# Performance work log

Measured on AMD Instinct MI355X. Metric: run time of the kernel, lower is better.

Reference implementation:

```python
import jax, jax.numpy as jnp
import numpy as np
import math

D = 256; H = 8; L = 6; DK = D // H

def _ln(x, g, b):
    m = jnp.mean(x, -1, keepdims=True)
    v = jnp.mean((x - m) ** 2, -1, keepdims=True)
    return (x - m) * jax.lax.rsqrt(v + 1e-5) * g + b

def setup_inputs() -> dict:
    key = jax.random.key(0)
    ks = jax.random.split(key, 16)
    B, N, F, E = 8, 768, 128, 4
    s = 0.02
    inp = {}
    inp['node_feats'] = jax.random.normal(ks[0], (B, N, F), jnp.float32)
    inp['adj'] = jax.random.randint(ks[1], (B, N, N), 0, 2, jnp.int32)
    inp['dist'] = jax.random.uniform(ks[2], (B, N, N), jnp.float32)
    inp['edge_type_oh'] = jax.random.uniform(ks[3], (B, N, N, E), jnp.float32)
    inp['node_proj_w'] = jax.random.normal(ks[4], (F, D), jnp.float32) * s
    inp['node_proj_b'] = jnp.zeros((D,), jnp.float32)
    inp['cls'] = jax.random.normal(ks[5], (1, 1, D), jnp.float32) * s
    inp['etw'] = jax.random.normal(ks[6], (E,), jnp.float32) * s
    inp['noedge_bias'] = jnp.float32(-2.0)
    inp['deg_scale'] = jnp.float32(0.2)
    inp['gamma'] = jnp.float32(0.8)
    inp['v2n'] = jnp.float32(0.1)
    inp['n2v'] = jnp.float32(0.1)
    inp['vself'] = jnp.float32(0.05)
    inp['ln1_g'] = jnp.ones((L, D), jnp.float32); inp['ln1_b'] = jnp.zeros((L, D), jnp.float32)
    inp['qw'] = jax.random.normal(ks[7], (L, D, D), jnp.float32) * s; inp['qb'] = jnp.zeros((L, D), jnp.float32)
    inp['kw'] = jax.random.normal(ks[8], (L, D, D), jnp.float32) * s; inp['kb'] = jnp.zeros((L, D), jnp.float32)
    inp['vw'] = jax.random.normal(ks[9], (L, D, D), jnp.float32) * s; inp['vb'] = jnp.zeros((L, D), jnp.float32)
    inp['ow'] = jax.random.normal(ks[10], (L, D, D), jnp.float32) * s; inp['ob'] = jnp.zeros((L, D), jnp.float32)
    inp['ln2_g'] = jnp.ones((L, D), jnp.float32); inp['ln2_b'] = jnp.zeros((L, D), jnp.float32)
    Dm = int(D * 1.0)  # mlp_ratio=1.0
    inp['fc1w'] = jax.random.normal(ks[11], (L, D, Dm), jnp.float32) * s; inp['fc1b'] = jnp.zeros((L, Dm), jnp.float32)
    inp['fc2w'] = jax.random.normal(ks[12], (L, Dm, D), jnp.float32) * s; inp['fc2b'] = jnp.zeros((L, D), jnp.float32)
    return inp

def _build_bias(adj_f, dist, edge_type_oh, etw, noedge_bias, deg_scale, gamma, v2n, n2v, vself):
    # DynamicAttnBiasBuilder: hard_mask=False, use_degree=True, vnode_spd_mode='replace', gamma != 0
    B, N, _ = adj_f.shape
    T = N + 1
    e = jnp.einsum('bije,e->bij', edge_type_oh, etw) - gamma * dist  # (B,N,N)
    e = jnp.where(adj_f > 0, e, e + noedge_bias)
    deg = adj_f.sum(-1)  # (B,N)
    deg_norm = (deg[:, :, None] + deg[:, None, :]) / (deg.max(axis=1, keepdims=True)[:, :, None] + 1e-6)
    e = e + deg_scale * deg_norm
    bias = jnp.zeros((B, T, T), jnp.float32)
    bias = bias.at[:, 1:, 1:].set(e)
    bias = bias.at[:, 0, 1:].set(v2n)   # vnode_spd_mode == 'replace'
    bias = bias.at[:, 1:, 0].set(n2v)
    bias = bias.at[:, 0, 0].set(vself)
    return bias  # (B,T,T), broadcast over heads

def _mhsa(x, bias, qw, qb, kw, kb, vw, vb, ow, ob):
    B, T, _ = x.shape
    q = (x @ qw + qb).reshape(B, T, H, DK).transpose(0, 2, 1, 3)
    k = (x @ kw + kb).reshape(B, T, H, DK).transpose(0, 2, 1, 3)
    v = (x @ vw + vb).reshape(B, T, H, DK).transpose(0, 2, 1, 3)
    scores = jnp.einsum('bhqd,bhkd->bhqk', q, k) / math.sqrt(DK)
    scores = scores + bias[:, None, :, :]
    attn = jax.nn.softmax(scores, axis=-1)
    out = jnp.einsum('bhqk,bhkd->bhqd', attn, v)
    out = out.transpose(0, 2, 1, 3).reshape(B, T, D)
    return out @ ow + ob

def _forward(node_feats, adj, dist, edge_type_oh, node_proj_w, node_proj_b, cls,
             etw, noedge_bias, deg_scale, gamma, v2n, n2v, vself,
             ln1_g, ln1_b, qw, qb, kw, kb, vw, vb, ow, ob,
             ln2_g, ln2_b, fc1w, fc1b, fc2w, fc2b):
    adj_f = adj.astype(jnp.float32)
    bias = _build_bias(adj_f, dist, edge_type_oh, etw, noedge_bias, deg_scale, gamma, v2n, n2v, vself)
    B = node_feats.shape[0]
    x = node_feats @ node_proj_w + node_proj_b  # (B,N,D)
    x = jnp.concatenate([jnp.broadcast_to(cls, (B, 1, D)), x], axis=1)  # prepend virtual node -> (B,T,D)
    for l in range(L):
        h = _mhsa(_ln(x, ln1_g[l], ln1_b[l]), bias, qw[l], qb[l], kw[l], kb[l], vw[l], vb[l], ow[l], ob[l])
        x = x + h
        m = _ln(x, ln2_g[l], ln2_b[l])
        m = jax.nn.gelu(m @ fc1w[l] + fc1b[l], approximate=False) @ fc2w[l] + fc2b[l]
        x = x + m
    return x

def reference(node_feats, adj, dist, edge_type_oh, node_proj_w, node_proj_b, cls,
              etw, noedge_bias, deg_scale, gamma, v2n, n2v, vself,
              ln1_g, ln1_b, qw, qb, kw, kb, vw, vb, ow, ob,
              ln2_g, ln2_b, fc1w, fc1b, fc2w, fc2b):
    return _forward(node_feats, adj, dist, edge_type_oh, node_proj_w, node_proj_b, cls,
                    etw, noedge_bias, deg_scale, gamma, v2n, n2v, vself,
                    ln1_g, ln1_b, qw, qb, kw, kb, vw, vb, ow, ob,
                    ln2_g, ln2_b, fc1w, fc1b, fc2w, fc2b)
```

## Files before the change

kernel.cpp:

```cpp
#include <hip/hip_runtime.h>
#include <math.h>

#define BB 8
#define NN 768
#define TT 769
#define DD 256
#define HH 8
#define DKK 32
#define FF 128
#define LL 6
#define MM 6152
#define SCALE 0.17677669529663687f
#define TP 832
#define KQP 784
#define KHS (KQP * DKK)
#define GBP 776
#define HP 264
#define WSZ 65536
#define NPK ((size_t)BB * 49 * 13 * 1024)

typedef __attribute__((ext_vector_type(8))) short s16x8;
typedef __attribute__((ext_vector_type(8))) unsigned short u16x8;
typedef __attribute__((ext_vector_type(4))) float f32x4;

__device__ inline short f2bf(float x) {
    unsigned u = __float_as_uint(x);
    unsigned r = (u + 0x7FFFu + ((u >> 16) & 1u)) >> 16;
    return (short)r;
}
__device__ inline float bf2f(unsigned short s) {
    return __uint_as_float(((unsigned)s) << 16);
}
__device__ inline float gelu_f(float x) {
    return 0.5f * x * (1.f + erff(x * 0.70710678118654752f));
}

__global__ __launch_bounds__(256) void deg_kernel(const int* __restrict__ adj,
                                                  float* __restrict__ deg) {
    int row  = blockIdx.x * 4 + (threadIdx.x >> 6);
    int lane = threadIdx.x & 63;
    const int* p = adj + (size_t)row * NN;
    int s = 0;
#pragma unroll
    for (int i = 0; i < NN / 64; ++i) s += p[lane + 64 * i];
#pragma unroll
    for (int off = 32; off > 0; off >>= 1) s += __shfl_xor(s, off);
    if (lane == 0) deg[row] = (float)s;
}

__global__ __launch_bounds__(256) void degmax_kernel(const float* __restrict__ deg,
                                                     float* __restrict__ dmax) {
    __shared__ float red[256];
    int b = blockIdx.x, t = threadIdx.x;
    float m = 0.f;
    for (int i = t; i < NN; i += 256) m = fmaxf(m, deg[b * NN + i]);
    red[t] = m;
    __syncthreads();
    for (int s = 128; s > 0; s >>= 1) {
        if (t < s) red[t] = fmaxf(red[t], red[t + s]);
        __syncthreads();
    }
    if (t == 0) dmax[b] = red[0];
}

__global__ __launch_bounds__(256) void bias_kernel(
    const float* __restrict__ dist, const float* __restrict__ eoh,
    const int* __restrict__ adj, const float* __restrict__ deg,
    const float* __restrict__ dmax, const float* __restrict__ etw,
    const float* __restrict__ noedge, const float* __restrict__ degsc,
    const float* __restrict__ gamma, const float* __restrict__ v2n,
    const float* __restrict__ n2v, const float* __restrict__ vself,
    unsigned short* __restrict__ bias)
{
    long long idx = (long long)blockIdx.x * 256 + threadIdx.x;
    const long long total = (long long)BB * TT * GBP;
    if (idx >= total) return;
    int b  = (int)(idx / ((long long)TT * GBP));
    int r  = (int)(idx % ((long long)TT * GBP));
    int qi = r / GBP, kj = r % GBP;
    float out;
    if (kj >= TT)                out = 0.f;
    else if (qi == 0 && kj == 0) out = vself[0];
    else if (qi == 0)            out = v2n[0];
    else if (kj == 0)            out = n2v[0];
    else {
        int i = qi - 1, j = kj - 1;
        size_t e = ((size_t)b * NN + i) * NN + j;
        float4 oh = *(const float4*)(eoh + 4 * e);
        float val = oh.x * etw[0] + oh.y * etw[1] + oh.z * etw[2] + oh.w * etw[3]
                    - gamma[0] * dist[e];
        if (adj[e] == 0) val += noedge[0];
        val += degsc[0] * (deg[b * NN + i] + deg[b * NN + j]) / (dmax[b] + 1e-6f);
        out = val;
    }
    bias[idx] = (unsigned short)f2bf(out);
}

__global__ __launch_bounds__(256) void biaspk_kernel(
    const unsigned short* __restrict__ bias, unsigned short* __restrict__ bpk)
{
    int idx = blockIdx.x * 256 + threadIdx.x;
    int jj   = idx & 7;
    int lane = (idx >> 3) & 63;
    int half = (idx >> 9) & 1;
    int c    = (idx >> 10) % 13;
    int qtb  = idx / (13 * 1024);
    int b = qtb / 49, qt = qtb - b * 49;
    int quad = lane >> 4, m16 = lane & 15;
    int j = half * 8 + jj, s = j >> 2, r = j & 3;
    int kj = c * 64 + s * 16 + m16; if (kj >= TT) kj = 0;
    int qi = qt * 16 + quad * 4 + r; if (qi >= TT) qi = TT - 1;
    bpk[idx] = bias[(size_t)(b * TT + qi) * GBP + kj];
}

__global__ __launch_bounds__(256) void nodeproj_ln_kernel(
    const float* __restrict__ nf, const float* __restrict__ w,
    const float* __restrict__ bsv, const float* __restrict__ cls,
    const float* __restrict__ g, const float* __restrict__ bvec,
    float* __restrict__ x, short* __restrict__ xn)
{
    __shared__ float sf[FF];
    __shared__ float red[256];
    int row = blockIdx.x, t = threadIdx.x;
    int b = row / TT, tr = row % TT;
    float y;
    if (tr == 0) {
        y = cls[t];
    } else {
        if (t < FF) sf[t] = nf[((size_t)b * NN + tr - 1) * FF + t];
        __syncthreads();
        y = bsv[t];
#pragma unroll 8
        for (int kk = 0; kk < FF; ++kk) y = fmaf(sf[kk], w[kk * DD + t], y);
    }
    x[(size_t)row * DD + t] = y;
    red[t] = y;
    __syncthreads();
    for (int s = 128; s > 0; s >>= 1) { if (t < s) red[t] += red[t + s]; __syncthreads(); }
    float mean = red[0] * (1.f / DD);
    __syncthreads();
    float d = y - mean;
    red[t] = d * d;
    __syncthreads();
    for (int s = 128; s > 0; s >>= 1) { if (t < s) red[t] += red[t + s]; __syncthreads(); }
    float var = red[0] * (1.f / DD);
    xn[(size_t)row * DD + t] = f2bf(d * rsqrtf(var + 1e-5f) * g[t] + bvec[t]);
}

__global__ __launch_bounds__(256) void wtrans_kernel(
    const float* __restrict__ qw, const float* __restrict__ kw,
    const float* __restrict__ vw, const float* __restrict__ ow,
    const float* __restrict__ f1w, const float* __restrict__ f2w,
    short* __restrict__ wt2)
{
    int mi = blockIdx.x >> 4, kg = blockIdx.x & 15;
    int fam = mi / 6, l = mi % 6;
    const float* W;
    if      (fam == 0) W = qw;
    else if (fam == 1) W = kw;
    else if (fam == 2) W = vw;
    else if (fam == 3) W = ow;
    else if (fam == 4) W = f1w;
    else               W = f2w;
    W += (size_t)l * DD * DD;
    int n = threadIdx.x;
    short* out = wt2 + (size_t)mi * WSZ;
#pragma unroll
    for (int kk = 0; kk < 16; ++kk) {
        int k = kg * 16 + kk;
        float val = W[(size_t)k * DD + n];
        size_t idx = (size_t)(((n >> 4) * 8 + (k >> 5)) * 512
                   + (((k >> 3) & 3) * 16 + (n & 15)) * 8 + (k & 7));
        out[idx] = f2bf(val);
    }
}

__global__ __launch_bounds__(256) void gemm_qkv_kernel(
    const short* __restrict__ A, const short* __restrict__ wtl,
    const float* __restrict__ qb, const float* __restrict__ kb,
    const float* __restrict__ vb,
    short* __restrict__ qh, short* __restrict__ kh, short* __restrict__ vtb)
{
    int t = threadIdx.x;
    int w = t >> 6, lane = t & 63, quad = lane >> 4, m16 = lane & 15;
    int m0 = blockIdx.x * 16;
    int fam = blockIdx.y;
    const short* Wf = wtl + (size_t)fam * 6 * WSZ;
    const float* bsv = fam == 0 ? qb : (fam == 1 ? kb : vb);
    int arow = m0 + m16; if (arow >= MM) arow = MM - 1;
    const short* ap = A + (size_t)arow * DD + quad * 8;
    const short* wbase = Wf + (size_t)(w * 4) * 4096 + lane * 8;
    f32x4 acc[4] = {};
#pragma unroll
    for (int kc = 0; kc < 8; ++kc) {
        s16x8 af = *(const s16x8*)(ap + kc * 32);
#pragma unroll
        for (int nt = 0; nt < 4; ++nt) {
            s16x8 bf = *(const s16x8*)(wbase + (size_t)nt * 4096 + kc * 512);
            acc[nt] = __builtin_amdgcn_mfma_f32_16x16x32_bf16(af, bf, acc[nt], 0, 0, 0);
        }
    }
    if (fam < 2) {
        short* outp = fam == 0 ? qh : kh;
#pragma unroll
        for (int r = 0; r < 4; ++r) {
            int row = m0 + quad * 4 + r;
            if (row < MM) {
                int b = row / TT;
                int tpos = row - b * TT;
                size_t rb = ((size_t)b * HH * KQP + tpos) * DKK;
#pragma unroll
                for (int nt = 0; nt < 4; ++nt) {
                    int col = w * 64 + nt * 16 + m16;
                    float bv = bsv[col];
                    int h = col >> 5, dk = col & 31;
                    outp[rb + (size_t)h * KHS + dk] = f2bf(acc[nt][r] + bv);
                }
            }
        }
    } else {
#pragma unroll
        for (int nt = 0; nt < 4; ++nt) {
            int col = w * 64 + nt * 16 + m16;
            float bv = bsv[col];
            int h = col >> 5, dk = col & 31;
#pragma unroll
            for (int r = 0; r < 4; ++r) {
                int row = m0 + quad * 4 + r;
                if (row < MM) {
                    int b = row / TT;
                    int tpos = row - b * TT;
                    vtb[(((size_t)(b * HH + h)) * DKK + dk) * TP + tpos] =
                        f2bf(acc[nt][r] + bv);
                }
            }
        }
    }
}

__global__ __launch_bounds__(512) void mega_kernel(
    const short* __restrict__ q, const short* __restrict__ k,
    const short* __restrict__ vt, const unsigned short* __restrict__ bpk,
    const short* __restrict__ Wo, const short* __restrict__ W1,
    const short* __restrict__ W2,
    const float* __restrict__ ob, const float* __restrict__ g2,
    const float* __restrict__ b2, const float* __restrict__ f1b,
    const float* __restrict__ f2b, float* __restrict__ x,
    short* __restrict__ xn, const float* __restrict__ g1,
    const float* __restrict__ b1, int donext)
{
    __shared__ short Pb[8][16][72];
    __shared__ short xa[16][HP];
    __shared__ short xnl[16][HP];
    __shared__ short hb[16][HP];
    __shared__ float redS[16][8], redQ[16][8];

    int t = threadIdx.x;
    int w = t >> 6, lane = t & 63;
    int quad = lane >> 4, m16 = lane & 15;
    int bx = blockIdx.x;
    int b = bx / 49;
    int qt = bx - b * 49;
    int h = w;
    int q0 = qt * 16;
    size_t qtb13 = (size_t)(b * 49 + qt) * 13;

    int qrow = q0 + m16;
    int qc = qrow < TT ? qrow : TT - 1;
    const short* qbase = q + (size_t)(b * HH + h) * KHS;
    s16x8 qa = *(const s16x8*)(qbase + (size_t)qc * DKK + quad * 8);

    const short* kbase = k + (size_t)(b * HH + h) * KHS;
    const short* vbase = vt + (((size_t)(b * HH + h)) * DKK) * TP;

    s16x8 kfA[4], kfB[4], vfA[4], vfB[4];
    u16x8 bbA0, bbA1, bbB0, bbB1;
    f32x4 sacc[4];
    f32x4 o0 = {0.f, 0.f, 0.f, 0.f};
    f32x4 o1 = {0.f, 0.f, 0.f, 0.f};
    float ls[4] = {0.f, 0.f, 0.f, 0.f};

#define LOADK_(DST, CC)                                                         \
    {                                                                           \
        _Pragma("unroll") for (int s = 0; s < 4; ++s) {                         \
            int kr = (CC) * 64 + s * 16 + m16;                                  \
            int kcl = kr < TT ? kr : TT - 1;                                    \
            DST[s] = *(const s16x8*)(kbase + (size_t)kcl * DKK + quad * 8);     \
        }                                                                       \
    }
#define LOADV_(DST, CC)                                                         \
    {                                                                           \
        int jn = (CC) * 64;                                                     \
        DST[0] = *(const s16x8*)(vbase + (size_t)m16 * TP + jn + quad * 8);     \
        DST[1] = *(const s16x8*)(vbase + (size_t)m16 * TP + jn + 32 + quad * 8);\
        DST[2] = *(const s16x8*)(vbase + (size_t)(16 + m16) * TP + jn + quad * 8);\
        DST[3] = *(const s16x8*)(vbase + (size_t)(16 + m16) * TP + jn + 32 + quad * 8);\
    }
#define LOADB_(D0, D1, CC)                                                      \
    {                                                                           \
        const unsigned short* bp_ = bpk + ((qtb13 + (CC)) << 10);               \
        D0 = *(const u16x8*)(bp_ + (lane << 3));                                \
        D1 = *(const u16x8*)(bp_ + 512 + (lane << 3));                          \
    }
#define STEP_(C, KPRE, KUSE, VUSE, VPRE, BU0, BU1, BP0, BP1, PK, PV, PBF, DOQK) \
    {                                                                           \
        if (PK)  LOADK_(KPRE, (C) + 2);                                         \
        if (PV)  LOADV_(VPRE, (C) + 1);                                         \
        if (PBF) LOADB_(BP0, BP1, (C) + 1);                                     \
        int j0 = (C) * 64;                                                      \
        _Pragma("unroll") for (int s = 0; s < 4; ++s) {                         \
            int key = j0 + s * 16 + m16;                                        \
            int kv = key < TT;                                                  \
            _Pragma("unroll") for (int r = 0; r < 4; ++r) {                     \
                int j = s * 4 + r;                                              \
                float bv = bf2f(j < 8 ? (unsigned short)BU0[j]                  \
                                      : (unsigned short)BU1[j - 8]);            \
                float sval = kv ? fmaf(sacc[s][r], SCALE, bv) : -1e30f;         \
                float p = __expf(sval - 8.0f);                                  \
                ls[r] += p;                                                     \
                Pb[w][quad * 4 + r][s * 16 + m16] = f2bf(p);                    \
            }                                                                   \
        }                                                                       \
        if (DOQK) {                                                             \
            f32x4 z = {0.f, 0.f, 0.f, 0.f};                                     \
            _Pragma("unroll") for (int s = 0; s < 4; ++s)                       \
                sacc[s] = __builtin_amdgcn_mfma_f32_16x16x32_bf16(qa, KUSE[s], z, 0, 0, 0); \
        }                                                                       \
        s16x8 pa0 = *(const s16x8*)&Pb[w][m16][quad * 8];                       \
        s16x8 pa1 = *(const s16x8*)&Pb[w][m16][32 + quad * 8];                  \
        o0 = __builtin_amdgcn_mfma_f32_16x16x32_bf16(pa0, VUSE[0], o0, 0, 0, 0);\
        o0 = __builtin_amdgcn_mfma_f32_16x16x32_bf16(pa1, VUSE[1], o0, 0, 0, 0);\
        o1 = __builtin_amdgcn_mfma_f32_16x16x32_bf16(pa0, VUSE[2], o1, 0, 0, 0);\
        o1 = __builtin_amdgcn_mfma_f32_16x16x32_bf16(pa1, VUSE[3], o1, 0, 0, 0);\
    }

    LOADK_(kfA, 0);
    LOADK_(kfB, 1);
    LOADV_(vfA, 0);
    LOADB_(bbA0, bbA1, 0);
    {
        f32x4 z = {0.f, 0.f, 0.f, 0.f};
#pragma unroll
        for (int s = 0; s < 4; ++s)
            sacc[s] = __builtin_amdgcn_mfma_f32_16x16x32_bf16(qa, kfA[s], z, 0, 0, 0);
    }

    for (int cc = 0; cc < 5; ++cc) {
        STEP_(2 * cc,     kfA, kfB, vfA, vfB, bbA0, bbA1, bbB0, bbB1, 1, 1, 1, 1)
        STEP_(2 * cc + 1, kfB, kfA, vfB, vfA, bbB0, bbB1, bbA0, bbA1, 1, 1, 1, 1)
    }
    STEP_(10, kfA, kfB, vfA, vfB, bbA0, bbA1, bbB0, bbB1, 1, 1, 1, 1)
    STEP_(11, kfB, kfA, vfB, vfA, bbB0, bbB1, bbA0, bbA1, 0, 1, 1, 1)
    STEP_(12, kfA, kfB, vfA, vfB, bbA0, bbA1, bbB0, bbB1, 0, 0, 0, 0)

#undef STEP_
#undef LOADB_
#undef LOADV_
#undef LOADK_

#pragma unroll
    for (int r = 0; r < 4; ++r) {
        float l = ls[r];
#pragma unroll
        for (int off = 1; off < 16; off <<= 1) l += __shfl_xor(l, off);
        float inv = 1.f / l;
        int rl = quad * 4 + r;
        xa[rl][h * DKK + m16]      = f2bf(o0[r] * inv);
        xa[rl][h * DKK + 16 + m16] = f2bf(o1[r] * inv);
    }
    __syncthreads();

    const short* wob = Wo + (size_t)(w * 2) * 4096 + lane * 8;
    f32x4 acco[2] = {};
#pragma unroll
    for (int kc = 0; kc < 8; ++kc) {
        s16x8 af = *(const s16x8*)&xa[m16][kc * 32 + quad * 8];
#pragma unroll
        for (int ntl = 0; ntl < 2; ++ntl) {
            s16x8 bf = *(const s16x8*)(wob + (size_t)ntl * 4096 + kc * 512);
            acco[ntl] = __builtin_amdgcn_mfma_f32_16x16x32_bf16(af, bf, acco[ntl], 0, 0, 0);
        }
    }
    float vv[2][4], sr[4], q2[4];
#pragma unroll
    for (int r = 0; r < 4; ++r) { sr[r] = 0.f; q2[r] = 0.f; }
#pragma unroll
    for (int ntl = 0; ntl < 2; ++ntl) {
        int col = w * 32 + ntl * 16 + m16;
        float bv = ob[col];
#pragma unroll
        for (int r = 0; r < 4; ++r) {
            int row = q0 + quad * 4 + r; if (row >= TT) row = TT - 1;
            float v = acco[ntl][r] + bv + x[((size_t)(b * TT + row)) * DD + col];
            vv[ntl][r] = v; sr[r] += v; q2[r] += v * v;
        }
    }
#pragma unroll
    for (int r = 0; r < 4; ++r)
#pragma unroll
        for (int off = 1; off < 16; off <<= 1) {
            sr[r] += __shfl_xor(sr[r], off);
            q2[r] += __shfl_xor(q2[r], off);
        }
    if (m16 == 0) {
#pragma unroll
        for (int r = 0; r < 4; ++r) {
            redS[quad * 4 + r][w] = sr[r];
            redQ[quad * 4 + r][w] = q2[r];
        }
    }
    __syncthreads();

#pragma unroll
    for (int r = 0; r < 4; ++r) {
        int rl = quad * 4 + r;
        float fs = 0.f, fq = 0.f;
#pragma unroll
        for (int j = 0; j < 8; ++j) { fs += redS[rl][j]; fq += redQ[rl][j]; }
        float mean = fs * (1.f / DD);
        float var = fq * (1.f / DD) - mean * mean;
        float inv = rsqrtf(var + 1e-5f);
#pragma unroll
        for (int ntl = 0; ntl < 2; ++ntl) {
            int col = w * 32 + ntl * 16 + m16;
            xnl[rl][col] = f2bf((vv[ntl][r] - mean) * inv * g2[col] + b2[col]);
        }
    }
    __syncthreads();

    const short* w1b = W1 + (size_t)(w * 2) * 4096 + lane * 8;
    f32x4 acc1[2] = {};
#pragma unroll
    for (int kc = 0; kc < 8; ++kc) {
        s16x8 af = *(const s16x8*)&xnl[m16][kc * 32 + quad * 8];
#pragma unroll
        for (int ntl = 0; ntl < 2; ++ntl) {
            s16x8 bf = *(const s16x8*)(w1b + (size_t)ntl * 4096 + kc * 512);
            acc1[ntl] = __builtin_amdgcn_mfma_f32_16x16x32_bf16(af, bf, acc1[ntl], 0, 0, 0);
        }
    }
#pragma unroll
    for (int ntl = 0; ntl < 2; ++ntl) {
        int col = w * 32 + ntl * 16 + m16;
        float fb = f1b[col];
#pragma unroll
        for (int r = 0; r < 4; ++r)
            hb[quad * 4 + r][col] = f2bf(gelu_f(acc1[ntl][r] + fb));
    }
    __syncthreads();

    const short* w2b = W2 + (size_t)(w * 2) * 4096 + lane * 8;
    f32x4 acc2[2] = {};
#pragma unroll
    for (int kc = 0; kc < 8; ++kc) {
        s16x8 af = *(const s16x8*)&hb[m16][kc * 32 + quad * 8];
#pragma unroll
        for (int ntl = 0; ntl < 2; ++ntl) {
            s16x8 bf = *(const s16x8*)(w2b + (size_t)ntl * 4096 + kc * 512);
            acc2[ntl] = __builtin_amdgcn_mfma_f32_16x16x32_bf16(af, bf, acc2[ntl], 0, 0, 0);
        }
    }
#pragma unroll
    for (int r = 0; r < 4; ++r) { sr[r] = 0.f; q2[r] = 0.f; }
#pragma unroll
    for (int ntl = 0; ntl < 2; ++ntl) {
        int col = w * 32 + ntl * 16 + m16;
        float bv = f2b[col];
#pragma unroll
        for (int r = 0; r < 4; ++r) {
            float v = acc2[ntl][r] + bv + vv[ntl][r];
            vv[ntl][r] = v; sr[r] += v; q2[r] += v * v;
        }
    }
#pragma unroll
    for (int r = 0; r < 4; ++r)
#pragma unroll
        for (int off = 1; off < 16; off <<= 1) {
            sr[r] += __shfl_xor(sr[r], off);
            q2[r] += __shfl_xor(q2[r], off);
        }
    if (m16 == 0) {
#pragma unroll
        for (int r = 0; r < 4; ++r) {
            redS[quad * 4 + r][w] = sr[r];
            redQ[quad * 4 + r][w] = q2[r];
        }
    }
    __syncthreads();

#pragma unroll
    for (int r = 0; r < 4; ++r) {
        int rl = quad * 4 + r;
        int row = q0 + rl;
        float fs = 0.f, fq = 0.f;
#pragma unroll
        for (int j = 0; j < 8; ++j) { fs += redS[rl][j]; fq += redQ[rl][j]; }
        float mean = fs * (1.f / DD);
        float var = fq * (1.f / DD) - mean * mean;
        float inv = rsqrtf(var + 1e-5f);
        if (row < TT) {
            size_t grow = (size_t)(b * TT + row) * DD;
#pragma unroll
            for (int ntl = 0; ntl < 2; ++ntl) {
                int col = w * 32 + ntl * 16 + m16;
                float v = vv[ntl][r];
                x[grow + col] = v;
                if (donext)
                    xn[grow + col] = f2bf((v - mean) * inv * g1[col] + b1[col]);
            }
        }
    }
}

extern "C" void kernel_launch(void* const* d_in, const int* in_sizes, int n_in,
                              void* d_out, int out_size, void* d_ws, size_t ws_size,
                              hipStream_t stream)
{
    const float* node_feats = (const float*)d_in[0];
    const int*   adj        = (const int*)d_in[1];
    const float* dist       = (const float*)d_in[2];
    const float* eoh        = (const float*)d_in[3];
    const float* npw        = (const float*)d_in[4];
    const float* npb        = (const float*)d_in[5];
    const float* cls        = (const float*)d_in[6];
    const float* etw        = (const float*)d_in[7];
    const float* noedge     = (const float*)d_in[8];
    const float* degsc      = (const float*)d_in[9];
    const float* gamma      = (const float*)d_in[10];
    const float* v2n        = (const float*)d_in[11];
    const float* n2v        = (const float*)d_in[12];
    const float* vself      = (const float*)d_in[13];
    const float* ln1g = (const float*)d_in[14];
    const float* ln1b = (const float*)d_in[15];
    const float* qw   = (const float*)d_in[16];
    const float* qb   = (const float*)d_in[17];
    const float* kw   = (const float*)d_in[18];
    const float* kb   = (const float*)d_in[19];
    const float* vw   = (const float*)d_in[20];
    const float* vb   = (const float*)d_in[21];
    const float* ow   = (const float*)d_in[22];
    const float* ob   = (const float*)d_in[23];
    const float* ln2g = (const float*)d_in[24];
    const float* ln2b = (const float*)d_in[25];
    const float* f1w  = (const float*)d_in[26];
    const float* f1b  = (const float*)d_in[27];
    const float* f2w  = (const float*)d_in[28];
    const float* f2b  = (const float*)d_in[29];

    float* x  = (float*)d_out;
    char* ws = (char*)d_ws;
    size_t off = 0;
    unsigned short* bias = (unsigned short*)(ws + off); off += (size_t)BB * TT * GBP * 2;
    unsigned short* bpk  = (unsigned short*)(ws + off); off += NPK * 2;
    float* deg  = (float*)(ws + off); off += (size_t)BB * NN * 4;
    float* dmax = (float*)(ws + off); off += 64;
    short* xn16 = (short*)(ws + off); off += (size_t)MM * DD * 2;
    short* qhb  = (short*)(ws + off); off += (size_t)BB * HH * KQP * DKK * 2;
    short* khb  = (short*)(ws + off); off += (size_t)BB * HH * KQP * DKK * 2;
    short* vtb  = (short*)(ws + off); off += (size_t)BB * HH * DKK * TP * 2;
    short* wt2  = (short*)(ws + off); off += (size_t)36 * WSZ * 2;

    deg_kernel<<<(BB * NN) / 4, 256, 0, stream>>>(adj, deg);
    degmax_kernel<<<BB, 256, 0, stream>>>(deg, dmax);

    long long total = (long long)BB * TT * GBP;
    bias_kernel<<<(int)((total + 255) / 256), 256, 0, stream>>>(
        dist, eoh, adj, deg, dmax, etw, noedge, degsc, gamma, v2n, n2v, vself, bias);

    biaspk_kernel<<<(int)(NPK / 256), 256, 0, stream>>>(bias, bpk);

    nodeproj_ln_kernel<<<MM, 256, 0, stream>>>(node_feats, npw, npb, cls,
                                               ln1g, ln1b, x, xn16);

    wtrans_kernel<<<576, 256, 0, stream>>>(qw, kw, vw, ow, f1w, f2w, wt2);

    dim3 gqkv(385, 3);
    for (int l = 0; l < LL; ++l) {
        size_t bo = (size_t)l * DD;
        gemm_qkv_kernel<<<gqkv, 256, 0, stream>>>(xn16, wt2 + (size_t)l * WSZ,
                                                  qb + bo, kb + bo, vb + bo,
                                                  qhb, khb, vtb);
        int donext = (l + 1 < LL) ? 1 : 0;
        size_t bn = (size_t)(l + 1 < LL ? l + 1 : 0) * DD;
        mega_kernel<<<392, 512, 0, stream>>>(
            qhb, khb, vtb, bpk,
            wt2 + (size_t)(3 * 6 + l) * WSZ,
            wt2 + (size_t)(4 * 6 + l) * WSZ,
            wt2 + (size_t)(5 * 6 + l) * WSZ,
            ob + bo, ln2g + bo, ln2b + bo, f1b + bo, f2b + bo,
            x, xn16, ln1g + bn, ln1b + bn, donext);
    }
}
```

Baseline: 671.8 us.

## Fuse next-layer QKV projection into mega kernel with ping-pong QKV buffers

Moves the next layer's LN1 and QKV projection into the tail of the mega kernel. Each block computes its 16-row tile's Q, K and V with MFMA from shared-memory normalized activations, writing into a second set of buffers that alternates between layers. This removes five separate QKV GEMM launches and the round trip of xn16 through global memory. It also remaps block indices so the batch index varies fastest. The cost is more work per block and extra shared-memory and register pressure in an already large kernel.

```diff
diff --git a/kernel.cpp b/kernel.cpp
--- a/kernel.cpp
+++ b/kernel.cpp
@@ -246,8 +246,13 @@
     const float* __restrict__ ob, const float* __restrict__ g2,
     const float* __restrict__ b2, const float* __restrict__ f1b,
     const float* __restrict__ f2b, float* __restrict__ x,
-    short* __restrict__ xn, const float* __restrict__ g1,
-    const float* __restrict__ b1, int donext)
+    const float* __restrict__ g1, const float* __restrict__ b1,
+    const short* __restrict__ Wq, const short* __restrict__ Wk,
+    const short* __restrict__ Wv,
+    const float* __restrict__ qbv, const float* __restrict__ kbv,
+    const float* __restrict__ vbv,
+    short* __restrict__ qho, short* __restrict__ kho,
+    short* __restrict__ vto, int donext)
 {
     __shared__ short Pb[8][16][72];
     __shared__ short xa[16][HP];
@@ -259,8 +264,8 @@
     int w = t >> 6, lane = t & 63;
     int quad = lane >> 4, m16 = lane & 15;
     int bx = blockIdx.x;
-    int b = bx / 49;
-    int qt = bx - b * 49;
+    int b = bx & 7;
+    int qt = bx >> 3;
     int h = w;
     int q0 = qt * 16;
     size_t qtb13 = (size_t)(b * 49 + qt) * 13;
@@ -300,7 +305,7 @@
     {                                                                           \
         const unsigned short* bp_ = bpk + ((qtb13 + (CC)) << 10);               \
         D0 = *(const u16x8*)(bp_ + (lane << 3));                                \
-        D1 = *(const u16x8*)(bp_ + 512 + (lane << 3));                          \
+        D1 = *(const u16x8*)(bp_ + 512 + (lane << 3));                         \
     }
 #define STEP_(C, KPRE, KUSE, VUSE, VPRE, BU0, BU1, BP0, BP1, PK, PV, PBF, DOQK) \
     {                                                                           \
@@ -498,15 +503,62 @@
         float mean = fs * (1.f / DD);
         float var = fq * (1.f / DD) - mean * mean;
         float inv = rsqrtf(var + 1e-5f);
-        if (row < TT) {
-            size_t grow = (size_t)(b * TT + row) * DD;
-#pragma unroll
-            for (int ntl = 0; ntl < 2; ++ntl) {
-                int col = w * 32 + ntl * 16 + m16;
-                float v = vv[ntl][r];
-                x[grow + col] = v;
-                if (donext)
-                    xn[grow + col] = f2bf((v - mean) * inv * g1[col] + b1[col]);
+        size_t grow = (size_t)(b * TT + (row < TT ? row : TT - 1)) * DD;
+#pragma unroll
+        for (int ntl = 0; ntl < 2; ++ntl) {
+            int col = w * 32 + ntl * 16 + m16;
+            float v = vv[ntl][r];
+            if (row < TT) x[grow + col] = v;
+            xa[rl][col] = f2bf((v - mean) * inv * g1[col] + b1[col]);
+        }
+    }
+
+    if (donext) {
+        __syncthreads();
+#pragma unroll
+        for (int fam = 0; fam < 3; ++fam) {
+            const short* Wf = fam == 0 ? Wq : (fam == 1 ? Wk : Wv);
+            const float* bsv = fam == 0 ? qbv : (fam == 1 ? kbv : vbv);
+            const short* wfb = Wf + (size_t)(w * 2) * 4096 + lane * 8;
+            f32x4 a3[2] = {};
+#pragma unroll
+            for (int kc = 0; kc < 8; ++kc) {
+                s16x8 af = *(const s16x8*)&xa[m16][kc * 32 + quad * 8];
+#pragma unroll
+                for (int ntl = 0; ntl < 2; ++ntl) {
+                    s16x8 bf = *(const s16x8*)(wfb + (size_t)ntl * 4096 + kc * 512);
+                    a3[ntl] = __builtin_amdgcn_mfma_f32_16x16x32_bf16(af, bf, a3[ntl], 0, 0, 0);
+                }
+            }
+            if (fam < 2) {
+                short* outp = fam == 0 ? qho : kho;
+#pragma unroll
+                for (int ntl = 0; ntl < 2; ++ntl) {
+                    int col = w * 32 + ntl * 16 + m16;
+                    float bv = bsv[col];
+                    int hh = col >> 5, dk = col & 31;
+#pragma unroll
+                    for (int r = 0; r < 4; ++r) {
+                        int row = q0 + quad * 4 + r;
+                        if (row < TT)
+                            outp[((size_t)b * HH * KQP + row) * DKK
+                                 + (size_t)hh * KHS + dk] = f2bf(a3[ntl][r] + bv);
+                    }
+                }
+            } else {
+#pragma unroll
+                for (int ntl = 0; ntl < 2; ++ntl) {
+                    int col = w * 32 + ntl * 16 + m16;
+                    float bv = bsv[col];
+                    int hh = col >> 5, dk = col & 31;
+#pragma unroll
+                    for (int r = 0; r < 4; ++r) {
+                        int row = q0 + quad * 4 + r;
+                        if (row < TT)
+                            vto[(((size_t)(b * HH + hh)) * DKK + dk) * TP + row] =
+                                f2bf(a3[ntl][r] + bv);
+                    }
+                }
             }
         }
     }
@@ -555,9 +607,13 @@
     float* deg  = (float*)(ws + off); off += (size_t)BB * NN * 4;
     float* dmax = (float*)(ws + off); off += 64;
     short* xn16 = (short*)(ws + off); off += (size_t)MM * DD * 2;
-    short* qhb  = (short*)(ws + off); off += (size_t)BB * HH * KQP * DKK * 2;
-    short* khb  = (short*)(ws + off); off += (size_t)BB * HH * KQP * DKK * 2;
-    short* vtb  = (short*)(ws + off); off += (size_t)BB * HH * DKK * TP * 2;
+    short* qhb[2]; short* khb[2]; short* vtb[2];
+    qhb[0] = (short*)(ws + off); off += (size_t)BB * HH * KQP * DKK * 2;
+    khb[0] = (short*)(ws + off); off += (size_t)BB * HH * KQP * DKK * 2;
+    vtb[0] = (short*)(ws + off); off += (size_t)BB * HH * DKK * TP * 2;
+    qhb[1] = (short*)(ws + off); off += (size_t)BB * HH * KQP * DKK * 2;
+    khb[1] = (short*)(ws + off); off += (size_t)BB * HH * KQP * DKK * 2;
+    vtb[1] = (short*)(ws + off); off += (size_t)BB * HH * DKK * TP * 2;
     short* wt2  = (short*)(ws + off); off += (size_t)36 * WSZ * 2;
 
     deg_kernel<<<(BB * NN) / 4, 256, 0, stream>>>(adj, deg);
@@ -575,19 +631,27 @@
     wtrans_kernel<<<576, 256, 0, stream>>>(qw, kw, vw, ow, f1w, f2w, wt2);
 
     dim3 gqkv(385, 3);
+    gemm_qkv_kernel<<<gqkv, 256, 0, stream>>>(xn16, wt2,
+                                              qb, kb, vb,
+                                              qhb[0], khb[0], vtb[0]);
+
     for (int l = 0; l < LL; ++l) {
         size_t bo = (size_t)l * DD;
-        gemm_qkv_kernel<<<gqkv, 256, 0, stream>>>(xn16, wt2 + (size_t)l * WSZ,
-                                                  qb + bo, kb + bo, vb + bo,
-                                                  qhb, khb, vtb);
         int donext = (l + 1 < LL) ? 1 : 0;
-        size_t bn = (size_t)(l + 1 < LL ? l + 1 : 0) * DD;
+        int ln = donext ? l + 1 : l;
+        size_t bn = (size_t)ln * DD;
+        int pi = l & 1, po = pi ^ 1;
         mega_kernel<<<392, 512, 0, stream>>>(
-            qhb, khb, vtb, bpk,
-            wt2 + (size_t)(3 * 6 + l) * WSZ,
-            wt2 + (size_t)(4 * 6 + l) * WSZ,
-            wt2 + (size_t)(5 * 6 + l) * WSZ,
+            qhb[pi], khb[pi], vtb[pi], bpk,
+            wt2 + (size_t)(18 + l) * WSZ,
+            wt2 + (size_t)(24 + l) * WSZ,
+            wt2 + (size_t)(30 + l) * WSZ,
             ob + bo, ln2g + bo, ln2b + bo, f1b + bo, f2b + bo,
-            x, xn16, ln1g + bn, ln1b + bn, donext);
-    }
-}
+            x, ln1g + bn, ln1b + bn,
+            wt2 + (size_t)(0 + ln) * WSZ,
+            wt2 + (size_t)(6 + ln) * WSZ,
+            wt2 + (size_t)(12 + ln) * WSZ,
+            qb + bn, kb + bn, vb + bn,
+            qhb[po], khb[po], vtb[po], donext);
+    }
+}
```

Result: slower. 703.6 us (+4.7%).
